# Kernel tuning notes

Hardware: AMD Instinct MI355X
Metric: run time of the kernel (lower is better)

Reference implementation:

```python
import jax, jax.numpy as jnp
import numpy as np
import math

HIDDEN = 1024
NUM_HEADS = 16
HEAD_DIM = 64
NUM_PREV = 4
BATCH = 4
SEQ = 1024
ROPE_BASE = 10000.0


def _rope(x):
    """Apply rotary embedding to x [..., seq, head_dim] (rotate-half form)."""
    d = x.shape[-1]
    s = x.shape[-2]
    inv_freq = 1.0 / (ROPE_BASE ** (jnp.arange(0, d, 2, dtype=jnp.float32) / d))
    ang = jnp.arange(s, dtype=jnp.float32)[:, None] * inv_freq[None, :]  # [s, d/2]
    cos, sin = jnp.cos(ang), jnp.sin(ang)
    x1, x2 = jnp.split(x, 2, axis=-1)
    return jnp.concatenate([x1 * cos - x2 * sin, x1 * sin + x2 * cos], axis=-1)


def setup_inputs() -> dict:
    key = jax.random.key(0)
    ks = jax.random.split(key, 8)
    std = 0.02
    d = {
        "hidden_states": jax.random.normal(ks[0], (BATCH, SEQ, HIDDEN), jnp.float32),
        "prev_hidden_states": jax.random.normal(ks[1], (NUM_PREV, BATCH, SEQ, HIDDEN), jnp.float32),
        "wq": jax.random.normal(ks[2], (HIDDEN, NUM_HEADS * HEAD_DIM), jnp.float32) * std,
        "bq": jnp.zeros((NUM_HEADS * HEAD_DIM,), jnp.float32),
        "wk": jax.random.normal(ks[3], (HIDDEN, NUM_HEADS * HEAD_DIM), jnp.float32) * std,
        "bk": jnp.zeros((NUM_HEADS * HEAD_DIM,), jnp.float32),
        "wv": jax.random.normal(ks[4], (HIDDEN, NUM_HEADS * HEAD_DIM), jnp.float32) * std,
        "bv": jnp.zeros((NUM_HEADS * HEAD_DIM,), jnp.float32),
        "wo": jax.random.normal(ks[5], (NUM_HEADS * HEAD_DIM, HIDDEN), jnp.float32) * std,
        "bo": jnp.zeros((HIDDEN,), jnp.float32),
        "wg": jax.random.normal(ks[6], (HIDDEN, NUM_PREV), jnp.float32) * std,
    }
    return d


def reference(hidden_states, prev_hidden_states, wq, bq, wk, bk, wv, bv, wo, bo, wg):
    B, S, H = hidden_states.shape
    P = prev_hidden_states.shape[0]
    nh, hd = NUM_HEADS, HEAD_DIM

    # Q projection + split heads + RoPE: [b, h, s, d]
    q = (hidden_states @ wq + bq).reshape(B, S, nh, hd).transpose(0, 2, 1, 3)
    q = _rope(q)

    # K/V projections for all prev layers at once: [p, b, h, s, d]
    k = (jnp.einsum('pbsh,he->pbse', prev_hidden_states, wk) + bk)
    k = k.reshape(P, B, S, nh, hd).transpose(0, 1, 3, 2, 4)
    k = _rope(k)
    v = (jnp.einsum('pbsh,he->pbse', prev_hidden_states, wv) + bv)
    v = v.reshape(P, B, S, nh, hd).transpose(0, 1, 3, 2, 4)

    # Attention per prev layer
    scale = 1.0 / math.sqrt(hd)
    attn = jnp.einsum('bhqd,pbhkd->pbhqk', q, k) * scale
    attn = jax.nn.softmax(attn, axis=-1)
    out = jnp.einsum('pbhqk,pbhkd->pbhqd', attn, v)  # [p, b, h, s, d]
    out = out.transpose(0, 1, 3, 2, 4).reshape(P, B, S, H)

    # Learned layer gating (faithful to original broadcast: requires B == P)
    pooled = jnp.mean(hidden_states, axis=1)            # [b, hidden]
    layer_w = jax.nn.softmax(pooled @ wg, axis=-1)      # [b, p]
    combined = jnp.sum(out * layer_w[:, :, None, None], axis=0)  # [b, s, hidden]

    return combined @ wo + bo
```

## Files before the change

kernel.cpp:

```cpp
#include <hip/hip_runtime.h>
#include <hip/hip_bf16.h>

#define B_  4
#define S_  1024
#define H_  1024
#define NH  16
#define HD  64
#define P_  4

typedef __attribute__((ext_vector_type(8))) short bf16x8;
typedef __attribute__((ext_vector_type(4))) float f32x4;

__device__ __forceinline__ float b2f(short s) {
  union { unsigned int u; float f; } v;
  v.u = ((unsigned int)(unsigned short)s) << 16;
  return v.f;
}
__device__ __forceinline__ short f2b(float f) {
  __hip_bfloat16 h = __float2bfloat16(f);
  return *reinterpret_cast<short*>(&h);
}
__device__ __forceinline__ float fast_exp2(float x) {
  float r;
  asm volatile("v_exp_f32 %0, %1" : "=v"(r) : "v"(x));
  return r;
}
__device__ __forceinline__ void gload_lds16(const void* g, void* l) {
  __builtin_amdgcn_global_load_lds(
      (const __attribute__((address_space(1))) unsigned int*)((uintptr_t)g),
      (__attribute__((address_space(3))) unsigned int*)((uintptr_t)l),
      16, 0, 0);
}

__global__ void prep_kernel(const float* __restrict__ hidden, const float* __restrict__ prev,
                            const float* __restrict__ wq, const float* __restrict__ wk,
                            const float* __restrict__ wv, const float* __restrict__ wo,
                            short* __restrict__ hbf, short* __restrict__ pbf,
                            short* __restrict__ wqT, short* __restrict__ wkT,
                            short* __restrict__ wvT, short* __restrict__ woT,
                            float* __restrict__ cost, float* __restrict__ sint,
                            float* __restrict__ pooled) {
  __shared__ short tile[32][33];
  int bid = blockIdx.x, tid = threadIdx.x;
  if (bid < 10240) {
    const float* src; short* dst; int idx;
    if (bid < 2048) { src = hidden; dst = hbf; idx = bid * 256 + tid; }
    else            { src = prev;   dst = pbf; idx = (bid - 2048) * 256 + tid; }
    const float4* s4 = (const float4*)(src + (size_t)idx * 8);
    float4 a = s4[0], b = s4[1];
    bf16x8 pk;
    pk[0] = f2b(a.x); pk[1] = f2b(a.y); pk[2] = f2b(a.z); pk[3] = f2b(a.w);
    pk[4] = f2b(b.x); pk[5] = f2b(b.y); pk[6] = f2b(b.z); pk[7] = f2b(b.w);
    *(bf16x8*)(dst + (size_t)idx * 8) = pk;
  } else if (bid < 14336) {
    int tb = bid - 10240;
    int z = tb >> 10, t = tb & 1023;
    const float* src = (z == 0) ? wq : (z == 1) ? wk : (z == 2) ? wv : wo;
    short*       dst = (z == 0) ? wqT : (z == 1) ? wkT : (z == 2) ? wvT : woT;
    int tx = tid & 31, ty = tid >> 5;
    int c0 = (t & 31) * 32, r0 = (t >> 5) * 32;
#pragma unroll
    for (int i = 0; i < 4; ++i)
      tile[ty + 8 * i][tx] = f2b(src[(r0 + ty + 8 * i) * 1024 + c0 + tx]);
    __syncthreads();
#pragma unroll
    for (int i = 0; i < 4; ++i)
      dst[(c0 + ty + 8 * i) * 1024 + r0 + tx] = tile[tx][ty + 8 * i];
  } else if (bid < 14464) {
    int idx = (bid - 14336) * 256 + tid;
    int s = idx >> 5, i = idx & 31;
    float invf = expf(-(float)i * (logf(10000.0f) / 32.0f));
    float a = (float)s * invf;
    cost[idx] = cosf(a);
    sint[idx] = sinf(a);
  } else {
    int idx = (bid - 14464) * 256 + tid;
    int b = idx >> 10, e = idx & 1023;
    const float* hp = hidden + (size_t)b * S_ * H_ + e;
    float s = 0.f;
    for (int t = 0; t < S_; ++t) s += hp[t * H_];
    pooled[idx] = s * (1.0f / 1024.0f);
  }
}

__global__ void gate_kernel(const float* __restrict__ pooled, const float* __restrict__ wg,
                            float* __restrict__ lw) {
  int w = threadIdx.x >> 6, lane = threadIdx.x & 63;
  float a0 = 0.f, a1 = 0.f, a2 = 0.f, a3 = 0.f;
  for (int e = lane; e < 1024; e += 64) {
    float pv = pooled[w * 1024 + e];
    a0 += pv * wg[e * 4 + 0];
    a1 += pv * wg[e * 4 + 1];
    a2 += pv * wg[e * 4 + 2];
    a3 += pv * wg[e * 4 + 3];
  }
#pragma unroll
  for (int off = 32; off > 0; off >>= 1) {
    a0 += __shfl_xor(a0, off, 64);
    a1 += __shfl_xor(a1, off, 64);
    a2 += __shfl_xor(a2, off, 64);
    a3 += __shfl_xor(a3, off, 64);
  }
  if (lane == 0) {
    float mx = fmaxf(fmaxf(a0, a1), fmaxf(a2, a3));
    float e0 = expf(a0 - mx), e1 = expf(a1 - mx), e2 = expf(a2 - mx), e3 = expf(a3 - mx);
    float inv = 1.0f / (e0 + e1 + e2 + e3);
    lw[w * 4 + 0] = e0 * inv;
    lw[w * 4 + 1] = e1 * inv;
    lw[w * 4 + 2] = e2 * inv;
    lw[w * 4 + 3] = e3 * inv;
  }
}

__device__ __forceinline__ void rope_epilogue(const f32x4 (&acc)[4][4], const float* __restrict__ bias,
                                              short* __restrict__ outp,
                                              const float* __restrict__ cost,
                                              const float* __restrict__ sint,
                                              int m0, int wm, int quad, int c, int hh) {
  float b0 = bias[hh * 64 + c];
  float b1 = bias[hh * 64 + 16 + c];
  float b2_ = bias[hh * 64 + 32 + c];
  float b3 = bias[hh * 64 + 48 + c];
#pragma unroll
  for (int mt = 0; mt < 4; ++mt) {
    int gm = m0 + wm * 64 + mt * 16 + quad * 4;
#pragma unroll
    for (int j = 0; j < 4; ++j) {
      int m = gm + j;
      int s = m & 1023;
      int bbx = m >> 10;
      int orow = ((bbx * NH + hh) * S_ + s) * HD;
      float c0f = cost[s * 32 + c], s0f = sint[s * 32 + c];
      float x1 = acc[mt][0][j] + b0, x2 = acc[mt][2][j] + b2_;
      outp[orow + c]      = f2b(x1 * c0f - x2 * s0f);
      outp[orow + 32 + c] = f2b(x1 * s0f + x2 * c0f);
      float c1f = cost[s * 32 + 16 + c], s1f = sint[s * 32 + 16 + c];
      float y1 = acc[mt][1][j] + b1, y2 = acc[mt][3][j] + b3;
      outp[orow + 16 + c] = f2b(y1 * c1f - y2 * s1f);
      outp[orow + 48 + c] = f2b(y1 * s1f + y2 * c1f);
    }
  }
}

__launch_bounds__(256, 2)
__global__ void qkv_gemm(const short* __restrict__ hbf, const short* __restrict__ pbf,
                         const short* __restrict__ BTq, const short* __restrict__ BTk,
                         const short* __restrict__ BTv,
                         const float* __restrict__ bq, const float* __restrict__ bk,
                         const float* __restrict__ bv,
                         short* __restrict__ outq, short* __restrict__ outk,
                         short* __restrict__ outv,
                         const float* __restrict__ cost, const float* __restrict__ sint) {
  __shared__ __align__(16) short As[128 * 32];
  __shared__ __align__(16) short Bs1[128 * 32];
  __shared__ __align__(16) short Bs2[128 * 32];
  int tid = threadIdx.x;
  int lane = tid & 63, wvv = tid >> 6;
  int quad = lane >> 4, c = lane & 15;
  int wm = wvv & 1, wn = wvv >> 1;
  bool isQ = blockIdx.y < 32;
  int m0 = (isQ ? blockIdx.y : (blockIdx.y - 32)) * 128;
  int n0 = blockIdx.x * 128;
  const short* A  = isQ ? hbf : pbf;
  const short* B1 = isQ ? BTq : BTk;
  f32x4 acc1[4][4] = {}, acc2[4][4] = {};
  const short* Ab = A + (size_t)m0 * 1024;
  const short* Bb1 = B1 + (size_t)n0 * 1024;
  const short* Bb2 = BTv + (size_t)n0 * 1024;
  int r1 = tid >> 2, c4a = (tid & 3) * 8;

  for (int kb = 0; kb < 32; ++kb) {
    int k0 = kb * 32;
    __syncthreads();
    gload_lds16(Ab + r1 * 1024 + k0 + c4a,         As + tid * 8);
    gload_lds16(Ab + (r1 + 64) * 1024 + k0 + c4a,  As + 2048 + tid * 8);
    gload_lds16(Bb1 + r1 * 1024 + k0 + c4a,        Bs1 + tid * 8);
    gload_lds16(Bb1 + (r1 + 64) * 1024 + k0 + c4a, Bs1 + 2048 + tid * 8);
    if (!isQ) {
      gload_lds16(Bb2 + r1 * 1024 + k0 + c4a,        Bs2 + tid * 8);
      gload_lds16(Bb2 + (r1 + 64) * 1024 + k0 + c4a, Bs2 + 2048 + tid * 8);
    }
    __syncthreads();
    bf16x8 af[4], b1f[4];
#pragma unroll
    for (int mt = 0; mt < 4; ++mt)
      af[mt] = *(const bf16x8*)&As[(wm * 64 + mt * 16 + c) * 32 + quad * 8];
#pragma unroll
    for (int nt = 0; nt < 4; ++nt)
      b1f[nt] = *(const bf16x8*)&Bs1[(wn * 64 + nt * 16 + c) * 32 + quad * 8];
#pragma unroll
    for (int mt = 0; mt < 4; ++mt)
#pragma unroll
      for (int nt = 0; nt < 4; ++nt)
        acc1[mt][nt] = __builtin_amdgcn_mfma_f32_16x16x32_bf16(af[mt], b1f[nt], acc1[mt][nt], 0, 0, 0);
    if (!isQ) {
      bf16x8 b2f_[4];
#pragma unroll
      for (int nt = 0; nt < 4; ++nt)
        b2f_[nt] = *(const bf16x8*)&Bs2[(wn * 64 + nt * 16 + c) * 32 + quad * 8];
#pragma unroll
      for (int mt = 0; mt < 4; ++mt)
#pragma unroll
        for (int nt = 0; nt < 4; ++nt)
          acc2[mt][nt] = __builtin_amdgcn_mfma_f32_16x16x32_bf16(af[mt], b2f_[nt], acc2[mt][nt], 0, 0, 0);
    }
  }

  int colb = n0 + wn * 64;
  int hh = colb >> 6;
  if (isQ) {
    rope_epilogue(acc1, bq, outq, cost, sint, m0, wm, quad, c, hh);
  } else {
    rope_epilogue(acc1, bk, outk, cost, sint, m0, wm, quad, c, hh);
    float bb[4];
#pragma unroll
    for (int nt = 0; nt < 4; ++nt) bb[nt] = bv[hh * 64 + nt * 16 + c];
#pragma unroll
    for (int mt = 0; mt < 4; ++mt) {
      int gm = m0 + wm * 64 + mt * 16 + quad * 4;
      int s4 = gm & 1023, pb = gm >> 10;
#pragma unroll
      for (int nt = 0; nt < 4; ++nt) {
        int d = nt * 16 + c;
        ushort4 pk;
        pk.x = (unsigned short)f2b(acc2[mt][nt][0] + bb[nt]);
        pk.y = (unsigned short)f2b(acc2[mt][nt][1] + bb[nt]);
        pk.z = (unsigned short)f2b(acc2[mt][nt][2] + bb[nt]);
        pk.w = (unsigned short)f2b(acc2[mt][nt][3] + bb[nt]);
        *(ushort4*)&outv[((pb * NH + hh) * HD + d) * S_ + s4] = pk;
      }
    }
  }
}

__launch_bounds__(256, 3)
__global__ void attn_kernel(const short* __restrict__ q, const short* __restrict__ k,
                            const short* __restrict__ vt, short* __restrict__ o) {
  int blk = blockIdx.x;
  int x = blk & 7, qt = (blk >> 3) & 7, g = blk >> 6;
  int pbh = g * 8 + x;
  int b = (pbh >> 4) & 3, h = pbh & 15;
  int tid = threadIdx.x;
  int w = tid >> 6, lane = tid & 63, quad = lane >> 4, c = lane & 15;
  int c7 = c & 7;

  __shared__ __align__(16) short Klds[64 * 64];
  __shared__ __align__(16) short Vlds[64 * 64];
  __shared__ __align__(16) short Plds[4][32 * 64];
  __shared__ float lsumf[4][32];

  const short* qbase = q + ((size_t)(b * NH + h) * S_ + qt * 128 + w * 32 + c) * HD;
  bf16x8 aq[2][2];
#pragma unroll
  for (int mi = 0; mi < 2; ++mi) {
    aq[mi][0] = *(const bf16x8*)(qbase + mi * 16 * HD + quad * 8);
    aq[mi][1] = *(const bf16x8*)(qbase + mi * 16 * HD + 32 + quad * 8);
  }

  const short* kb = k + (size_t)pbh * S_ * HD;
  const short* vb = vt + (size_t)pbh * HD * S_;

  f32x4 O[2][4] = {};
  float lsum[2] = {0.f, 0.f};
  const float cs = 0.18033688011f;

  int sr = tid >> 3;
  int lc = (tid & 7) ^ (sr & 7);

  for (int kt = 0; kt < 16; ++kt) {
    __syncthreads();
    const short* ksrc = kb + (kt * 64 + sr) * HD + lc * 8;
    gload_lds16(ksrc,           Klds + tid * 8);
    gload_lds16(ksrc + 32 * HD, Klds + 2048 + tid * 8);
    const short* vsrc = vb + (size_t)sr * S_ + kt * 64 + lc * 8;
    gload_lds16(vsrc,           Vlds + tid * 8);
    gload_lds16(vsrc + 32 * S_, Vlds + 2048 + tid * 8);
    __syncthreads();

    bf16x8 kf[4][2];
#pragma unroll
    for (int t = 0; t < 4; ++t) {
      int row = (t * 16 + c) * 64;
      kf[t][0] = *(const bf16x8*)&Klds[row + (quad ^ c7) * 8];
      kf[t][1] = *(const bf16x8*)&Klds[row + (quad ^ 4 ^ c7) * 8];
    }

#pragma unroll
    for (int mi = 0; mi < 2; ++mi) {
      int rq = mi * 16 + c;
#pragma unroll
      for (int t = 0; t < 4; ++t) {
        f32x4 st = {};
        st = __builtin_amdgcn_mfma_f32_16x16x32_bf16(kf[t][0], aq[mi][0], st, 0, 0, 0);
        st = __builtin_amdgcn_mfma_f32_16x16x32_bf16(kf[t][1], aq[mi][1], st, 0, 0, 0);
        short4 pk4;
        float p0 = fast_exp2(st[0] * cs);
        float p1 = fast_exp2(st[1] * cs);
        float p2 = fast_exp2(st[2] * cs);
        float p3 = fast_exp2(st[3] * cs);
        lsum[mi] += (p0 + p1) + (p2 + p3);
        pk4.x = f2b(p0); pk4.y = f2b(p1); pk4.z = f2b(p2); pk4.w = f2b(p3);
        int chunkL = t * 2 + (quad >> 1);
        *(short4*)&Plds[w][rq * 64 + ((chunkL ^ c7)) * 8 + (quad & 1) * 4] = pk4;
      }
    }

    bf16x8 bv0[4], bv1[4];
#pragma unroll
    for (int nt = 0; nt < 4; ++nt) {
      int row = (nt * 16 + c) * 64;
      bv0[nt] = *(const bf16x8*)&Vlds[row + (quad ^ c7) * 8];
      bv1[nt] = *(const bf16x8*)&Vlds[row + (quad ^ 4 ^ c7) * 8];
    }
#pragma unroll
    for (int mi = 0; mi < 2; ++mi) {
      int prow = (mi * 16 + c) * 64;
      bf16x8 aP0 = *(const bf16x8*)&Plds[w][prow + (quad ^ c7) * 8];
      bf16x8 aP1 = *(const bf16x8*)&Plds[w][prow + (quad ^ 4 ^ c7) * 8];
#pragma unroll
      for (int nt = 0; nt < 4; ++nt) {
        O[mi][nt] = __builtin_amdgcn_mfma_f32_16x16x32_bf16(aP0, bv0[nt], O[mi][nt], 0, 0, 0);
        O[mi][nt] = __builtin_amdgcn_mfma_f32_16x16x32_bf16(aP1, bv1[nt], O[mi][nt], 0, 0, 0);
      }
    }
  }

#pragma unroll
  for (int mi = 0; mi < 2; ++mi) {
    float s = lsum[mi];
    s += __shfl_xor(s, 16, 64);
    s += __shfl_xor(s, 32, 64);
    if (lane < 16) lsumf[w][mi * 16 + c] = s;
  }
#pragma unroll
  for (int mi = 0; mi < 2; ++mi) {
    f32x4 lv = *(const f32x4*)&lsumf[w][mi * 16 + quad * 4];
    short* ob = o + ((size_t)pbh * S_ + qt * 128 + w * 32 + mi * 16 + quad * 4) * HD;
#pragma unroll
    for (int j = 0; j < 4; ++j) {
      float inv = 1.0f / lv[j];
      ob[j * HD + c]      = f2b(O[mi][0][j] * inv);
      ob[j * HD + 16 + c] = f2b(O[mi][1][j] * inv);
      ob[j * HD + 32 + c] = f2b(O[mi][2][j] * inv);
      ob[j * HD + 48 + c] = f2b(O[mi][3][j] * inv);
    }
  }
}

__global__ void combine_kernel(const short* __restrict__ o, const float* __restrict__ lw,
                               short* __restrict__ comb) {
  int idx = blockIdx.x * 256 + threadIdx.x;
  int e8 = idx & 127;
  int s = (idx >> 7) & 1023;
  int b = idx >> 17;
  int h = e8 >> 3, d0 = (e8 & 7) * 8;
  float acc[8] = {};
#pragma unroll
  for (int p = 0; p < 4; ++p) {
    float wgt = lw[p * 4 + b];
    const short* op = o + (((size_t)(p * 4 + b) * NH + h) * S_ + s) * HD + d0;
    bf16x8 v = *(const bf16x8*)op;
#pragma unroll
    for (int i = 0; i < 8; ++i) acc[i] += wgt * b2f(v[i]);
  }
  bf16x8 pk;
#pragma unroll
  for (int i = 0; i < 8; ++i) pk[i] = f2b(acc[i]);
  *(bf16x8*)&comb[((size_t)b * S_ + s) * H_ + e8 * 8] = pk;
}

__launch_bounds__(256, 4)
__global__ void gemm_out(const short* __restrict__ A, const short* __restrict__ BT,
                         const float* __restrict__ bias, float* __restrict__ outf) {
  __shared__ __align__(16) short As[64 * 32];
  __shared__ __align__(16) short Bs[128 * 32];
  int tid = threadIdx.x;
  int lane = tid & 63, wvv = tid >> 6;
  int quad = lane >> 4, c = lane & 15;
  int wm = wvv & 1, wn = wvv >> 1;
  int m0 = blockIdx.y * 64, n0 = blockIdx.x * 128;
  f32x4 acc[2][4] = {};
  const short* Ab = A + (size_t)m0 * 1024;
  const short* Bb = BT + (size_t)n0 * 1024;
  int r1 = tid >> 2, c4a = (tid & 3) * 8;

  for (int kb = 0; kb < 32; ++kb) {
    int k0 = kb * 32;
    __syncthreads();
    gload_lds16(Ab + r1 * 1024 + k0 + c4a,        As + tid * 8);
    gload_lds16(Bb + r1 * 1024 + k0 + c4a,        Bs + tid * 8);
    gload_lds16(Bb + (r1 + 64) * 1024 + k0 + c4a, Bs + 2048 + tid * 8);
    __syncthreads();
    bf16x8 af[2], bfr[4];
#pragma unroll
    for (int mt = 0; mt < 2; ++mt)
      af[mt] = *(const bf16x8*)&As[(wm * 32 + mt * 16 + c) * 32 + quad * 8];
#pragma unroll
    for (int nt = 0; nt < 4; ++nt)
      bfr[nt] = *(const bf16x8*)&Bs[(wn * 64 + nt * 16 + c) * 32 + quad * 8];
#pragma unroll
    for (int mt = 0; mt < 2; ++mt)
#pragma unroll
      for (int nt = 0; nt < 4; ++nt)
        acc[mt][nt] = __builtin_amdgcn_mfma_f32_16x16x32_bf16(af[mt], bfr[nt], acc[mt][nt], 0, 0, 0);
  }

  int colb = n0 + wn * 64;
  float bb[4];
#pragma unroll
  for (int nt = 0; nt < 4; ++nt) bb[nt] = bias[colb + nt * 16 + c];
#pragma unroll
  for (int mt = 0; mt < 2; ++mt) {
    int gm = m0 + wm * 32 + mt * 16 + quad * 4;
#pragma unroll
    for (int j = 0; j < 4; ++j) {
      int m = gm + j;
#pragma unroll
      for (int nt = 0; nt < 4; ++nt)
        outf[(size_t)m * 1024 + colb + nt * 16 + c] = acc[mt][nt][j] + bb[nt];
    }
  }
}

extern "C" void kernel_launch(void* const* d_in, const int* in_sizes, int n_in,
                              void* d_out, int out_size, void* d_ws, size_t ws_size,
                              hipStream_t stream) {
  (void)in_sizes; (void)n_in; (void)out_size; (void)ws_size;
  const float* hidden = (const float*)d_in[0];
  const float* prev   = (const float*)d_in[1];
  const float* wq = (const float*)d_in[2];
  const float* bq = (const float*)d_in[3];
  const float* wk = (const float*)d_in[4];
  const float* bk = (const float*)d_in[5];
  const float* wv = (const float*)d_in[6];
  const float* bv = (const float*)d_in[7];
  const float* wo = (const float*)d_in[8];
  const float* bo = (const float*)d_in[9];
  const float* wg = (const float*)d_in[10];
  float* out = (float*)d_out;
  char* ws = (char*)d_ws;

  size_t off = 0;
  short* wqT = (short*)(ws + off); off += (size_t)1024 * 1024 * 2;
  short* wkT = (short*)(ws + off); off += (size_t)1024 * 1024 * 2;
  short* wvT = (short*)(ws + off); off += (size_t)1024 * 1024 * 2;
  short* woT = (short*)(ws + off); off += (size_t)1024 * 1024 * 2;
  short* hbf = (short*)(ws + off); off += (size_t)B_ * S_ * H_ * 2;
  short* pbf = (short*)(ws + off); off += (size_t)P_ * B_ * S_ * H_ * 2;
  short* qbf = (short*)(ws + off); off += (size_t)B_ * S_ * H_ * 2;
  short* kbf = (short*)(ws + off); off += (size_t)P_ * B_ * S_ * H_ * 2;
  short* vtb = (short*)(ws + off); off += (size_t)P_ * B_ * S_ * H_ * 2;
  float* cost = (float*)(ws + off); off += (size_t)S_ * 32 * 4;
  float* sint = (float*)(ws + off); off += (size_t)S_ * 32 * 4;
  float* pooled = (float*)(ws + off); off += (size_t)B_ * H_ * 4;
  float* lw = (float*)(ws + off); off += 64;
  short* obf  = pbf;
  short* comb = qbf;

  prep_kernel<<<14480, 256, 0, stream>>>(hidden, prev, wq, wk, wv, wo,
                                         hbf, pbf, wqT, wkT, wvT, woT,
                                         cost, sint, pooled);
  gate_kernel<<<1, 256, 0, stream>>>(pooled, wg, lw);
  qkv_gemm<<<dim3(8, 160), 256, 0, stream>>>(hbf, pbf, wqT, wkT, wvT,
                                             bq, bk, bv, qbf, kbf, vtb, cost, sint);
  attn_kernel<<<2048, 256, 0, stream>>>(qbf, kbf, vtb, obf);
  combine_kernel<<<2048, 256, 0, stream>>>(obf, lw, comb);
  gemm_out<<<dim3(8, 64), 256, 0, stream>>>(comb, woT, bo, out);
}
```

Before: 405.8 us.

## Double K-tile depth, swizzle LDS, and remap blocks per XCD in GEMMs

Both the QKV and output GEMMs now load 64-wide K slices per iteration instead of 32, which halves the number of barrier pairs. The LDS layout is XOR-swizzled by row to avoid bank conflicts on fragment reads. A 1D grid is remapped so each XCD gets a contiguous M-row group sharing the same A tiles, aiming for better L2 reuse. LDS use doubles, which may limit occupancy, especially for qkv_gemm at 48KB per block.

After: 375.7 us. -7.4%, faster.

```diff
diff --git a/kernel.cpp b/kernel.cpp
--- a/kernel.cpp
+++ b/kernel.cpp
@@ -151,58 +151,73 @@
                          short* __restrict__ outq, short* __restrict__ outk,
                          short* __restrict__ outv,
                          const float* __restrict__ cost, const float* __restrict__ sint) {
-  __shared__ __align__(16) short As[128 * 32];
-  __shared__ __align__(16) short Bs1[128 * 32];
-  __shared__ __align__(16) short Bs2[128 * 32];
+  __shared__ __align__(16) short As[128 * 64];
+  __shared__ __align__(16) short Bs1[128 * 64];
+  __shared__ __align__(16) short Bs2[128 * 64];
+  int id = blockIdx.x;
+  int xcd = id & 7;
+  int local = id >> 3;
+  int n0i = local & 7;
+  int yl = local >> 3;
+  int y = yl * 8 + xcd;
   int tid = threadIdx.x;
   int lane = tid & 63, wvv = tid >> 6;
   int quad = lane >> 4, c = lane & 15;
   int wm = wvv & 1, wn = wvv >> 1;
-  bool isQ = blockIdx.y < 32;
-  int m0 = (isQ ? blockIdx.y : (blockIdx.y - 32)) * 128;
-  int n0 = blockIdx.x * 128;
+  bool isQ = y < 32;
+  int m0 = (isQ ? y : (y - 32)) * 128;
+  int n0 = n0i * 128;
   const short* A  = isQ ? hbf : pbf;
   const short* B1 = isQ ? BTq : BTk;
   f32x4 acc1[4][4] = {}, acc2[4][4] = {};
   const short* Ab = A + (size_t)m0 * 1024;
   const short* Bb1 = B1 + (size_t)n0 * 1024;
   const short* Bb2 = BTv + (size_t)n0 * 1024;
-  int r1 = tid >> 2, c4a = (tid & 3) * 8;
-
-  for (int kb = 0; kb < 32; ++kb) {
-    int k0 = kb * 32;
-    __syncthreads();
-    gload_lds16(Ab + r1 * 1024 + k0 + c4a,         As + tid * 8);
-    gload_lds16(Ab + (r1 + 64) * 1024 + k0 + c4a,  As + 2048 + tid * 8);
-    gload_lds16(Bb1 + r1 * 1024 + k0 + c4a,        Bs1 + tid * 8);
-    gload_lds16(Bb1 + (r1 + 64) * 1024 + k0 + c4a, Bs1 + 2048 + tid * 8);
-    if (!isQ) {
-      gload_lds16(Bb2 + r1 * 1024 + k0 + c4a,        Bs2 + tid * 8);
-      gload_lds16(Bb2 + (r1 + 64) * 1024 + k0 + c4a, Bs2 + 2048 + tid * 8);
-    }
-    __syncthreads();
-    bf16x8 af[4], b1f[4];
-#pragma unroll
-    for (int mt = 0; mt < 4; ++mt)
-      af[mt] = *(const bf16x8*)&As[(wm * 64 + mt * 16 + c) * 32 + quad * 8];
-#pragma unroll
-    for (int nt = 0; nt < 4; ++nt)
-      b1f[nt] = *(const bf16x8*)&Bs1[(wn * 64 + nt * 16 + c) * 32 + quad * 8];
-#pragma unroll
-    for (int mt = 0; mt < 4; ++mt)
-#pragma unroll
-      for (int nt = 0; nt < 4; ++nt)
-        acc1[mt][nt] = __builtin_amdgcn_mfma_f32_16x16x32_bf16(af[mt], b1f[nt], acc1[mt][nt], 0, 0, 0);
-    if (!isQ) {
-      bf16x8 b2f_[4];
-#pragma unroll
-      for (int nt = 0; nt < 4; ++nt)
-        b2f_[nt] = *(const bf16x8*)&Bs2[(wn * 64 + nt * 16 + c) * 32 + quad * 8];
+  int sr = tid >> 3, sch = tid & 7;
+
+  for (int kb = 0; kb < 16; ++kb) {
+    int k0 = kb * 64;
+    __syncthreads();
+#pragma unroll
+    for (int rd = 0; rd < 4; ++rd) {
+      int row = sr + rd * 32;
+      int col = ((sch ^ (row & 7)) * 8) + k0;
+      gload_lds16(Ab + row * 1024 + col,  As  + rd * 2048 + tid * 8);
+      gload_lds16(Bb1 + row * 1024 + col, Bs1 + rd * 2048 + tid * 8);
+      if (!isQ) gload_lds16(Bb2 + row * 1024 + col, Bs2 + rd * 2048 + tid * 8);
+    }
+    __syncthreads();
+#pragma unroll
+    for (int ko = 0; ko < 2; ++ko) {
+      bf16x8 af[4], b1f[4];
+#pragma unroll
+      for (int mt = 0; mt < 4; ++mt) {
+        int row = wm * 64 + mt * 16 + c;
+        af[mt] = *(const bf16x8*)&As[row * 64 + (((ko * 4 + quad) ^ (row & 7)) * 8)];
+      }
+#pragma unroll
+      for (int nt = 0; nt < 4; ++nt) {
+        int row = wn * 64 + nt * 16 + c;
+        b1f[nt] = *(const bf16x8*)&Bs1[row * 64 + (((ko * 4 + quad) ^ (row & 7)) * 8)];
+      }
 #pragma unroll
       for (int mt = 0; mt < 4; ++mt)
 #pragma unroll
         for (int nt = 0; nt < 4; ++nt)
-          acc2[mt][nt] = __builtin_amdgcn_mfma_f32_16x16x32_bf16(af[mt], b2f_[nt], acc2[mt][nt], 0, 0, 0);
+          acc1[mt][nt] = __builtin_amdgcn_mfma_f32_16x16x32_bf16(af[mt], b1f[nt], acc1[mt][nt], 0, 0, 0);
+      if (!isQ) {
+        bf16x8 b2f_[4];
+#pragma unroll
+        for (int nt = 0; nt < 4; ++nt) {
+          int row = wn * 64 + nt * 16 + c;
+          b2f_[nt] = *(const bf16x8*)&Bs2[row * 64 + (((ko * 4 + quad) ^ (row & 7)) * 8)];
+        }
+#pragma unroll
+        for (int mt = 0; mt < 4; ++mt)
+#pragma unroll
+          for (int nt = 0; nt < 4; ++nt)
+            acc2[mt][nt] = __builtin_amdgcn_mfma_f32_16x16x32_bf16(af[mt], b2f_[nt], acc2[mt][nt], 0, 0, 0);
+      }
     }
   }
 
@@ -372,37 +387,59 @@
 __launch_bounds__(256, 4)
 __global__ void gemm_out(const short* __restrict__ A, const short* __restrict__ BT,
                          const float* __restrict__ bias, float* __restrict__ outf) {
-  __shared__ __align__(16) short As[64 * 32];
-  __shared__ __align__(16) short Bs[128 * 32];
+  __shared__ __align__(16) short As[64 * 64];
+  __shared__ __align__(16) short Bs[128 * 64];
+  int id = blockIdx.x;
+  int xcd = id & 7;
+  int local = id >> 3;
+  int n0i = local & 7;
+  int yl = local >> 3;
+  int y = yl * 8 + xcd;
   int tid = threadIdx.x;
   int lane = tid & 63, wvv = tid >> 6;
   int quad = lane >> 4, c = lane & 15;
   int wm = wvv & 1, wn = wvv >> 1;
-  int m0 = blockIdx.y * 64, n0 = blockIdx.x * 128;
+  int m0 = y * 64, n0 = n0i * 128;
   f32x4 acc[2][4] = {};
   const short* Ab = A + (size_t)m0 * 1024;
   const short* Bb = BT + (size_t)n0 * 1024;
-  int r1 = tid >> 2, c4a = (tid & 3) * 8;
-
-  for (int kb = 0; kb < 32; ++kb) {
-    int k0 = kb * 32;
-    __syncthreads();
-    gload_lds16(Ab + r1 * 1024 + k0 + c4a,        As + tid * 8);
-    gload_lds16(Bb + r1 * 1024 + k0 + c4a,        Bs + tid * 8);
-    gload_lds16(Bb + (r1 + 64) * 1024 + k0 + c4a, Bs + 2048 + tid * 8);
-    __syncthreads();
-    bf16x8 af[2], bfr[4];
-#pragma unroll
-    for (int mt = 0; mt < 2; ++mt)
-      af[mt] = *(const bf16x8*)&As[(wm * 32 + mt * 16 + c) * 32 + quad * 8];
-#pragma unroll
-    for (int nt = 0; nt < 4; ++nt)
-      bfr[nt] = *(const bf16x8*)&Bs[(wn * 64 + nt * 16 + c) * 32 + quad * 8];
-#pragma unroll
-    for (int mt = 0; mt < 2; ++mt)
-#pragma unroll
-      for (int nt = 0; nt < 4; ++nt)
-        acc[mt][nt] = __builtin_amdgcn_mfma_f32_16x16x32_bf16(af[mt], bfr[nt], acc[mt][nt], 0, 0, 0);
+  int sr = tid >> 3, sch = tid & 7;
+
+  for (int kb = 0; kb < 16; ++kb) {
+    int k0 = kb * 64;
+    __syncthreads();
+#pragma unroll
+    for (int rd = 0; rd < 2; ++rd) {
+      int row = sr + rd * 32;
+      int col = ((sch ^ (row & 7)) * 8) + k0;
+      gload_lds16(Ab + row * 1024 + col, As + rd * 2048 + tid * 8);
+    }
+#pragma unroll
+    for (int rd = 0; rd < 4; ++rd) {
+      int row = sr + rd * 32;
+      int col = ((sch ^ (row & 7)) * 8) + k0;
+      gload_lds16(Bb + row * 1024 + col, Bs + rd * 2048 + tid * 8);
+    }
+    __syncthreads();
+#pragma unroll
+    for (int ko = 0; ko < 2; ++ko) {
+      bf16x8 af[2], bfr[4];
+#pragma unroll
+      for (int mt = 0; mt < 2; ++mt) {
+        int row = wm * 32 + mt * 16 + c;
+        af[mt] = *(const bf16x8*)&As[row * 64 + (((ko * 4 + quad) ^ (row & 7)) * 8)];
+      }
+#pragma unroll
+      for (int nt = 0; nt < 4; ++nt) {
+        int row = wn * 64 + nt * 16 + c;
+        bfr[nt] = *(const bf16x8*)&Bs[row * 64 + (((ko * 4 + quad) ^ (row & 7)) * 8)];
+      }
+#pragma unroll
+      for (int mt = 0; mt < 2; ++mt)
+#pragma unroll
+        for (int nt = 0; nt < 4; ++nt)
+          acc[mt][nt] = __builtin_amdgcn_mfma_f32_16x16x32_bf16(af[mt], bfr[nt], acc[mt][nt], 0, 0, 0);
+    }
   }
 
   int colb = n0 + wn * 64;
@@ -461,9 +498,9 @@
                                          hbf, pbf, wqT, wkT, wvT, woT,
                                          cost, sint, pooled);
   gate_kernel<<<1, 256, 0, stream>>>(pooled, wg, lw);
-  qkv_gemm<<<dim3(8, 160), 256, 0, stream>>>(hbf, pbf, wqT, wkT, wvT,
-                                             bq, bk, bv, qbf, kbf, vtb, cost, sint);
+  qkv_gemm<<<1280, 256, 0, stream>>>(hbf, pbf, wqT, wkT, wvT,
+                                     bq, bk, bv, qbf, kbf, vtb, cost, sint);
   attn_kernel<<<2048, 256, 0, stream>>>(qbf, kbf, vtb, obf);
   combine_kernel<<<2048, 256, 0, stream>>>(obf, lw, comb);
-  gemm_out<<<dim3(8, 64), 256, 0, stream>>>(comb, woT, bo, out);
-}
+  gemm_out<<<512, 256, 0, stream>>>(comb, woT, bo, out);
+}
```
